# Optimization experiments

Measured on AMD Instinct MI355X. Metric: run time of the kernel, lower is better.

The kernel has to match this reference:

```python
import jax, jax.numpy as jnp
import numpy as np

B, S, D, H, F = 4, 2048, 1024, 16, 4096
HD = D // H
EPS = 1e-6
ROPE_BASE = 10000.0


def apply_rope(x, positions, head_dim):
    # x: [B, S, H, hd], positions: [B, S]
    fraction = 2.0 * jnp.arange(0, head_dim // 2, dtype=jnp.float32) / head_dim
    timescale = ROPE_BASE ** fraction                      # [hd/2]
    angle = positions[:, :, None, None].astype(jnp.float32) / timescale  # [B,S,1,hd/2]
    sin, cos = jnp.sin(angle), jnp.cos(angle)
    first, second = jnp.split(x, 2, axis=-1)
    return jnp.concatenate([first * cos - second * sin,
                            second * cos + first * sin], axis=-1).astype(x.dtype)


def rms_norm(x, scale):
    var = jnp.mean(jnp.square(x), axis=-1, keepdims=True)
    return (x * jax.lax.rsqrt(var + EPS)) * scale


def setup_inputs() -> dict:
    key = jax.random.key(0)
    ks = jax.random.split(key, 10)
    std = 0.02
    x = jax.random.normal(ks[0], (B, S, D), dtype=jnp.float32)
    segment_positions = jnp.broadcast_to(jnp.arange(S, dtype=jnp.int32), (B, S))
    mask = jnp.broadcast_to(jnp.tril(jnp.ones((S, S), dtype=bool))[None, None], (B, 1, S, S))
    wq = jax.random.normal(ks[1], (D, H, HD), dtype=jnp.float32) * std
    wk = jax.random.normal(ks[2], (D, H, HD), dtype=jnp.float32) * std
    wv = jax.random.normal(ks[3], (D, H, HD), dtype=jnp.float32) * std
    wo = jax.random.normal(ks[4], (H, HD, D), dtype=jnp.float32) * std
    w_gate = jax.random.normal(ks[5], (D, F), dtype=jnp.float32) * std
    w_up = jax.random.normal(ks[6], (D, F), dtype=jnp.float32) * std
    w_down = jax.random.normal(ks[7], (F, D), dtype=jnp.float32) * std
    norm1 = jnp.ones((D,), dtype=jnp.float32)
    norm2 = jnp.ones((D,), dtype=jnp.float32)
    return dict(x=x, segment_positions=segment_positions, mask=mask,
                wq=wq, wk=wk, wv=wv, wo=wo,
                w_gate=w_gate, w_up=w_up, w_down=w_down,
                norm1=norm1, norm2=norm2)


def reference(x, segment_positions, mask, wq, wk, wv, wo, w_gate, w_up, w_down, norm1, norm2):
    # --- pre-norm RoPE attention residual block ---
    h = rms_norm(x, norm1)                                  # [B,S,D]
    q = jnp.einsum('bsd,dhk->bshk', h, wq)                  # [B,S,H,hd]
    k = jnp.einsum('bsd,dhk->bshk', h, wk)
    v = jnp.einsum('bsd,dhk->bshk', h, wv)
    q = apply_rope(q, segment_positions, HD)
    k = apply_rope(k, segment_positions, HD)
    q = q / jnp.sqrt(jnp.float32(HD))
    attn = jnp.einsum('bqhd,bkhd->bhqk', q, k)              # [B,H,S,S]
    big_neg = jnp.finfo(jnp.float32).min
    attn = jnp.where(mask, attn, big_neg)
    attn = jax.nn.softmax(attn, axis=-1)
    ctx = jnp.einsum('bhqk,bkhd->bqhd', attn, v)            # [B,S,H,hd]
    x = x + jnp.einsum('bqhd,hdo->bqo', ctx, wo)            # residual
    # --- pre-norm GLU FFN residual block ---
    h = rms_norm(x, norm2)
    gated = jax.nn.gelu(h @ w_gate) * (h @ w_up)            # [B,S,F]
    x = x + gated @ w_down
    return x
```

## Files before the change

kernel.cpp:

```cpp
#include <hip/hip_runtime.h>
#include <cstdint>
#include <cstddef>

#define BQ 4
#define SQ 2048
#define DQ 1024
#define HQ 16
#define HDQ 64
#define FQ 4096
#define MROWS (BQ * SQ)

typedef __attribute__((ext_vector_type(8))) __bf16 bf16x8;
typedef __attribute__((ext_vector_type(8))) unsigned short u16x8;
typedef __attribute__((ext_vector_type(4))) float f32x4;

__device__ __forceinline__ unsigned short f2bf(float f) {
  unsigned int u = __builtin_bit_cast(unsigned int, f);
  u = (u + 0x7FFFu + ((u >> 16) & 1u)) >> 16;
  return (unsigned short)u;
}
__device__ __forceinline__ float bf2f(unsigned short h) {
  unsigned int u = ((unsigned int)h) << 16;
  return __builtin_bit_cast(float, u);
}

typedef const unsigned int __attribute__((address_space(1))) *as1_cu32;
typedef unsigned int __attribute__((address_space(3))) *as3_u32;
#define GLD16(g, l) __builtin_amdgcn_global_load_lds((as1_cu32)(const void*)(g), (as3_u32)(void*)(l), 16, 0, 0)

__global__ __launch_bounds__(256) void k_transpose_bf16(const float* __restrict__ src,
                                                        unsigned short* __restrict__ dst,
                                                        int R, int C) {
  __shared__ float tile[32][33];
  int tx = threadIdx.x & 31, ty = threadIdx.x >> 5;
  int c0 = blockIdx.x * 32, r0 = blockIdx.y * 32;
#pragma unroll
  for (int i = 0; i < 32; i += 8)
    tile[ty + i][tx] = src[(size_t)(r0 + ty + i) * C + (c0 + tx)];
  __syncthreads();
#pragma unroll
  for (int i = 0; i < 32; i += 8)
    dst[(size_t)(c0 + ty + i) * R + (r0 + tx)] = f2bf(tile[tx][ty + i]);
}

__global__ __launch_bounds__(256) void k_rmsnorm(const float* __restrict__ x,
                                                 const float* __restrict__ g,
                                                 unsigned short* __restrict__ out) {
  int row = blockIdx.x, tid = threadIdx.x;
  const float4 v = ((const float4*)(x + (size_t)row * DQ))[tid];
  float ss = v.x * v.x + v.y * v.y + v.z * v.z + v.w * v.w;
#pragma unroll
  for (int d = 32; d >= 1; d >>= 1) ss += __shfl_xor(ss, d);
  __shared__ float ws4[4];
  if ((tid & 63) == 0) ws4[tid >> 6] = ss;
  __syncthreads();
  float tot = ws4[0] + ws4[1] + ws4[2] + ws4[3];
  float r = rsqrtf(tot * (1.0f / DQ) + 1e-6f);
  const float4 gv = ((const float4*)g)[tid];
  ushort4 o;
  o.x = f2bf(v.x * r * gv.x);
  o.y = f2bf(v.y * r * gv.y);
  o.z = f2bf(v.z * r * gv.z);
  o.w = f2bf(v.w * r * gv.w);
  ((ushort4*)(out + (size_t)row * DQ))[tid] = o;
}

template <int MODE>
__global__ __launch_bounds__(256) void k_gemm_bt(const unsigned short* __restrict__ A,
                                                 const unsigned short* __restrict__ Bt,
                                                 void* __restrict__ Cp,
                                                 const float* __restrict__ Res,
                                                 int M, int N, int K) {
  __shared__ __align__(16) unsigned short As[128 * 32];
  __shared__ __align__(16) unsigned short Bs[128 * 32];
  const int tid = threadIdx.x;
  const int lane = tid & 63, w = tid >> 6;
  const int m0 = blockIdx.y * 128, n0 = blockIdx.x * 128;
  const int wm = (w >> 1) * 64, wn = (w & 1) * 64;
  const int lr = lane & 15, lg = lane >> 4;
  f32x4 acc[4][4] = {};
  for (int k0 = 0; k0 < K; k0 += 32) {
#pragma unroll
    for (int i = 0; i < 2; ++i) {
      int flat = i * 256 + tid;
      int row = flat >> 2, ch = flat & 3;
      GLD16(A + (size_t)(m0 + row) * K + k0 + ch * 8, As + (size_t)(i * 256 + w * 64) * 8);
      GLD16(Bt + (size_t)(n0 + row) * K + k0 + ch * 8, Bs + (size_t)(i * 256 + w * 64) * 8);
    }
    __syncthreads();
    bf16x8 af[4], bfr[4];
#pragma unroll
    for (int mi = 0; mi < 4; ++mi)
      af[mi] = *(const bf16x8*)(As + (wm + mi * 16 + lr) * 32 + lg * 8);
#pragma unroll
    for (int ni = 0; ni < 4; ++ni)
      bfr[ni] = *(const bf16x8*)(Bs + (wn + ni * 16 + lr) * 32 + lg * 8);
#pragma unroll
    for (int mi = 0; mi < 4; ++mi)
#pragma unroll
      for (int ni = 0; ni < 4; ++ni)
        acc[mi][ni] = __builtin_amdgcn_mfma_f32_16x16x32_bf16(af[mi], bfr[ni], acc[mi][ni], 0, 0, 0);
    __syncthreads();
  }
#pragma unroll
  for (int mi = 0; mi < 4; ++mi) {
#pragma unroll
    for (int r = 0; r < 4; ++r) {
      int gr = m0 + wm + mi * 16 + lg * 4 + r;
#pragma unroll
      for (int ni = 0; ni < 4; ++ni) {
        int gc = n0 + wn + ni * 16 + lr;
        size_t idx = (size_t)gr * N + gc;
        float v = acc[mi][ni][r];
        if (MODE == 0) {
          ((unsigned short*)Cp)[idx] = f2bf(v);
        } else if (MODE == 1) {
          ((float*)Cp)[idx] = v + Res[idx];
        } else {
          float u = bf2f(((unsigned short*)Cp)[idx]);
          float t = v + 0.044715f * v * v * v;
          float gl = 0.5f * v * (1.0f + tanhf(0.7978845608028654f * t));
          ((unsigned short*)Cp)[idx] = f2bf(gl * u);
        }
      }
    }
  }
}

template <int MODE>
__global__ __launch_bounds__(512, 2) void k_gemm256(const unsigned short* __restrict__ A,
                                                    const unsigned short* __restrict__ Bt,
                                                    void* __restrict__ Cp,
                                                    int M, int N, int K) {
  __shared__ __align__(16) unsigned short Ab[2][2][128 * 64];
  __shared__ __align__(16) unsigned short Bb[2][2][128 * 64];
  const int tid = threadIdx.x, lane = tid & 63, w = tid >> 6;
  const int nwg = (int)gridDim.x;
  const int nx = N >> 8;
  const int cpx = nwg >> 3;
  const int bid = (int)blockIdx.x;
  const int swz = (bid & 7) * cpx + (bid >> 3);
  const int bx = swz % nx, by = swz / nx;
  const int m0 = by * 256, n0 = bx * 256;
  const int wr = (w >> 2) * 128, wc = (w & 3) * 64;
  const int lr = lane & 15, lg = lane >> 4;
  const int NT = K >> 6;
  const int r0 = tid >> 3;
  const int c0sw = (tid & 7) ^ (r0 & 7);
  f32x4 acc[8][4] = {};

#define BAR() asm volatile("s_barrier" ::: "memory")

#define STG(isB, hh_, t_)                                                         \
  do {                                                                            \
    int tpar = (t_) & 1;                                                          \
    int t2 = (t_) > NT - 1 ? NT - 1 : (t_);                                       \
    const unsigned short* gb = (isB) ? Bt : A;                                    \
    int rb = ((isB) ? n0 : m0) + (hh_) * 128;                                     \
    unsigned short* lb =                                                          \
        ((isB) ? &Bb[tpar][hh_][0] : &Ab[tpar][hh_][0]) + (size_t)(w * 64) * 8;   \
    const unsigned short* g0 = gb + (size_t)(rb + r0) * K + t2 * 64 + c0sw * 8;   \
    GLD16(g0, lb);                                                                \
    GLD16(g0 + (size_t)64 * K, lb + 512 * 8);                                     \
  } while (0)

#define RD_A(dst, MH, par)                                                        \
  _Pragma("unroll") for (int mi2 = 0; mi2 < 4; ++mi2) {                           \
    int rr = (wr + ((MH)*4 + mi2) * 16 + lr) & 127;                               \
    int hh = wr >> 7;                                                             \
    _Pragma("unroll") for (int ks = 0; ks < 2; ++ks)                              \
        dst[mi2][ks] =                                                            \
        *(const bf16x8*)&Ab[par][hh][rr * 64 + (((ks * 4 + lg) ^ (rr & 7)) * 8)]; \
  }

#define RD_B(dst, NH, par)                                                        \
  _Pragma("unroll") for (int ni2 = 0; ni2 < 2; ++ni2) {                           \
    int c256 = wc + ((NH)*2 + ni2) * 16 + lr;                                     \
    int hh = c256 >> 7, rr = c256 & 127;                                          \
    _Pragma("unroll") for (int ks = 0; ks < 2; ++ks)                              \
        dst[ni2][ks] =                                                            \
        *(const bf16x8*)&Bb[par][hh][rr * 64 + (((ks * 4 + lg) ^ (rr & 7)) * 8)]; \
  }

#define MM(MH, NH, aqv, bqv)                                                      \
  _Pragma("unroll") for (int mi2 = 0; mi2 < 4; ++mi2)                             \
  _Pragma("unroll") for (int ni2 = 0; ni2 < 2; ++ni2)                             \
  _Pragma("unroll") for (int ks = 0; ks < 2; ++ks)                                \
      acc[(MH)*4 + mi2][(NH)*2 + ni2] = __builtin_amdgcn_mfma_f32_16x16x32_bf16(  \
          aqv[mi2][ks], bqv[ni2][ks], acc[(MH)*4 + mi2][(NH)*2 + ni2], 0, 0, 0);

  STG(0, 0, 0);
  STG(0, 1, 0);
  STG(1, 0, 0);
  STG(1, 1, 0);
  STG(1, 0, 1);
  STG(1, 1, 1);
  asm volatile("s_waitcnt vmcnt(4)" ::: "memory");
  BAR();

  for (int kt = 0; kt < NT; ++kt) {
    const int p = kt & 1;
    bf16x8 aq[4][2], bq0[2][2], bq1[2][2];
    RD_A(aq, 0, p);
    RD_B(bq0, 0, p);
    STG(0, 0, kt + 1);
    BAR();
    __builtin_amdgcn_s_setprio(1);
    MM(0, 0, aq, bq0);
    __builtin_amdgcn_s_setprio(0);
    BAR();
    RD_B(bq1, 1, p);
    STG(0, 1, kt + 1);
    BAR();
    __builtin_amdgcn_s_setprio(1);
    MM(0, 1, aq, bq1);
    __builtin_amdgcn_s_setprio(0);
    BAR();
    RD_A(aq, 1, p);
    STG(1, 0, kt + 2);
    BAR();
    __builtin_amdgcn_s_setprio(1);
    MM(1, 1, aq, bq1);
    __builtin_amdgcn_s_setprio(0);
    BAR();
    STG(1, 1, kt + 2);
    asm volatile("s_waitcnt vmcnt(4)" ::: "memory");
    BAR();
    __builtin_amdgcn_s_setprio(1);
    MM(1, 0, aq, bq0);
    __builtin_amdgcn_s_setprio(0);
    BAR();
  }
  asm volatile("s_waitcnt vmcnt(0)" ::: "memory");
#pragma unroll
  for (int mi = 0; mi < 8; ++mi) {
#pragma unroll
    for (int r = 0; r < 4; ++r) {
      int gr = m0 + wr + mi * 16 + lg * 4 + r;
#pragma unroll
      for (int ni = 0; ni < 4; ++ni) {
        int gc = n0 + wc + ni * 16 + lr;
        size_t idx = (size_t)gr * N + gc;
        float v = acc[mi][ni][r];
        if (MODE == 0) {
          ((unsigned short*)Cp)[idx] = f2bf(v);
        } else {
          float u = bf2f(((unsigned short*)Cp)[idx]);
          float t = v + 0.044715f * v * v * v;
          float gl = 0.5f * v * (1.0f + tanhf(0.7978845608028654f * t));
          ((unsigned short*)Cp)[idx] = f2bf(gl * u);
        }
      }
    }
  }
#undef BAR
#undef STG
#undef RD_A
#undef RD_B
#undef MM
}

__global__ __launch_bounds__(256) void k_rope(const unsigned short* __restrict__ qkv,
                                              const int* __restrict__ pos,
                                              unsigned short* __restrict__ qp,
                                              unsigned short* __restrict__ kp,
                                              unsigned short* __restrict__ vpT) {
  __shared__ unsigned short T[64 * 67];
  const float NEG_L2TS = -0.4152410118609203f;
  const float QSCALE = 0.125f * 1.4426950408889634f;
  int bh = blockIdx.y, b = bh >> 4, hh = bh & 15;
  int s0 = blockIdx.x * 64;
  int tid = threadIdx.x;
  int row = tid >> 2, q4 = tid & 3, j0 = q4 * 8;
  int gs = s0 + row;
  const unsigned short* base = qkv + ((size_t)(b * SQ + gs)) * 3072 + hh * 64;
  u16x8 q1 = *(const u16x8*)(base + j0);
  u16x8 q2 = *(const u16x8*)(base + 32 + j0);
  u16x8 k1 = *(const u16x8*)(base + 1024 + j0);
  u16x8 k2 = *(const u16x8*)(base + 1024 + 32 + j0);
  u16x8 v1 = *(const u16x8*)(base + 2048 + j0);
  u16x8 v2 = *(const u16x8*)(base + 2048 + 32 + j0);
  float fp = (float)pos[b * SQ + gs];
  u16x8 oq1, oq2, ok1, ok2;
#pragma unroll
  for (int jj = 0; jj < 8; ++jj) {
    float ang = fp * exp2f((float)(j0 + jj) * NEG_L2TS);
    float sn, cs;
    __sincosf(ang, &sn, &cs);
    float q1f = bf2f(q1[jj]), q2f = bf2f(q2[jj]);
    float k1f = bf2f(k1[jj]), k2f = bf2f(k2[jj]);
    oq1[jj] = f2bf((q1f * cs - q2f * sn) * QSCALE);
    oq2[jj] = f2bf((q2f * cs + q1f * sn) * QSCALE);
    ok1[jj] = f2bf(k1f * cs - k2f * sn);
    ok2[jj] = f2bf(k2f * cs + k1f * sn);
    T[row * 67 + j0 + jj] = v1[jj];
    T[row * 67 + 32 + j0 + jj] = v2[jj];
  }
  size_t o = ((size_t)bh * SQ + gs) * 64;
  *(u16x8*)(qp + o + j0) = oq1;
  *(u16x8*)(qp + o + 32 + j0) = oq2;
  *(u16x8*)(kp + o + j0) = ok1;
  *(u16x8*)(kp + o + 32 + j0) = ok2;
  __syncthreads();
  int hd = tid >> 2;
#pragma unroll
  for (int c2 = 0; c2 < 2; ++c2) {
    int sb = q4 * 16 + c2 * 8;
    u16x8 ov;
#pragma unroll
    for (int ii = 0; ii < 8; ++ii) ov[ii] = T[(sb + ii) * 67 + hd];
    *(u16x8*)(vpT + ((size_t)bh * 64 + hd) * SQ + s0 + sb) = ov;
  }
}

__global__ __launch_bounds__(256) void k_flash(const unsigned short* __restrict__ qp,
                                               const unsigned short* __restrict__ kp,
                                               const unsigned short* __restrict__ vpT,
                                               unsigned short* __restrict__ ctx) {
  __shared__ __align__(16) unsigned short Ks[2][64 * 64];
  __shared__ __align__(16) unsigned short Vs[2][64 * 64];
  __shared__ __align__(16) unsigned short Ps[4][16 * 64];
  int qb = 31 - (int)blockIdx.x;
  int bh = blockIdx.y, b = bh >> 4, hh = bh & 15;
  int tid = threadIdx.x, lane = tid & 63, w = tid >> 6;
  const int lr = lane & 15, lg = lane >> 4;
  const int key = lr & 7;
  size_t hoff = (size_t)bh * SQ * 64;
  const unsigned short* Q = qp + hoff;
  const unsigned short* Kg = kp + hoff;
  const unsigned short* Vh = vpT + hoff;
  int qr0 = qb * 64 + w * 16;
  bf16x8 aq0 = *(const bf16x8*)(Q + (size_t)(qr0 + lr) * 64 + lg * 8);
  bf16x8 aq1 = *(const bf16x8*)(Q + (size_t)(qr0 + lr) * 64 + 32 + lg * 8);
  f32x4 accO[4] = {};
  float mrow[4] = {-1e30f, -1e30f, -1e30f, -1e30f};
  float lrow[4] = {0.f, 0.f, 0.f, 0.f};
  int nt = qb + 1;

#define STAGE(d, t)                                                              \
  {                                                                              \
    int kv0s = (t) * 64;                                                         \
    _Pragma("unroll") for (int i = 0; i < 2; ++i) {                              \
      int flat = i * 256 + tid;                                                  \
      int srow = flat >> 3;                                                      \
      int ch = (flat & 7) ^ (srow & 7);                                          \
      GLD16(Kg + (size_t)(kv0s + srow) * 64 + ch * 8, &Ks[d][(i * 256 + w * 64) * 8]); \
      GLD16(Vh + (size_t)srow * SQ + kv0s + ch * 8, &Vs[d][(i * 256 + w * 64) * 8]);   \
    }                                                                            \
  }

  STAGE(0, 0);
  __syncthreads();
  for (int t = 0; t < nt; ++t) {
    int kv0 = t * 64;
    if (t + 1 < nt) STAGE((t + 1) & 1, t + 1);
    const unsigned short* Kc = Ks[t & 1];
    const unsigned short* Vc = Vs[t & 1];
    f32x4 sacc[4] = {};
#pragma unroll
    for (int nh = 0; nh < 4; ++nh) {
      const unsigned short* kr = Kc + (nh * 16 + lr) * 64;
      bf16x8 b0 = *(const bf16x8*)(kr + (lg ^ key) * 8);
      bf16x8 b1 = *(const bf16x8*)(kr + ((lg + 4) ^ key) * 8);
      sacc[nh] = __builtin_amdgcn_mfma_f32_16x16x32_bf16(aq0, b0, sacc[nh], 0, 0, 0);
      sacc[nh] = __builtin_amdgcn_mfma_f32_16x16x32_bf16(aq1, b1, sacc[nh], 0, 0, 0);
    }
    bool diag = (t == qb);
    float scl[4];
#pragma unroll
    for (int i = 0; i < 4; ++i) {
      float s0 = sacc[0][i], s1 = sacc[1][i], s2 = sacc[2][i], s3 = sacc[3][i];
      if (diag) {
        int gr = qr0 + lg * 4 + i;
        int c = kv0 + lr;
        if (c > gr) s0 = -1e30f;
        if (c + 16 > gr) s1 = -1e30f;
        if (c + 32 > gr) s2 = -1e30f;
        if (c + 48 > gr) s3 = -1e30f;
      }
      float mt = fmaxf(fmaxf(s0, s1), fmaxf(s2, s3));
      mt = fmaxf(mt, __shfl_xor(mt, 1));
      mt = fmaxf(mt, __shfl_xor(mt, 2));
      mt = fmaxf(mt, __shfl_xor(mt, 4));
      mt = fmaxf(mt, __shfl_xor(mt, 8));
      float mnew = fmaxf(mrow[i], mt);
      scl[i] = exp2f(mrow[i] - mnew);
      mrow[i] = mnew;
      float p0 = exp2f(s0 - mnew), p1 = exp2f(s1 - mnew);
      float p2 = exp2f(s2 - mnew), p3 = exp2f(s3 - mnew);
      lrow[i] = lrow[i] * scl[i] + (p0 + p1 + p2 + p3);
      int prow = lg * 4 + i;
      unsigned short* Pr = &Ps[w][prow * 64];
      int pk = prow & 7;
      int sub = lr >> 3, off = lr & 7;
      Pr[((0 + sub) ^ pk) * 8 + off] = f2bf(p0);
      Pr[((2 + sub) ^ pk) * 8 + off] = f2bf(p1);
      Pr[((4 + sub) ^ pk) * 8 + off] = f2bf(p2);
      Pr[((6 + sub) ^ pk) * 8 + off] = f2bf(p3);
    }
#pragma unroll
    for (int n2 = 0; n2 < 4; ++n2)
#pragma unroll
      for (int i = 0; i < 4; ++i) accO[n2][i] *= scl[i];
    bf16x8 ap0 = *(const bf16x8*)(&Ps[w][lr * 64] + (lg ^ key) * 8);
    bf16x8 ap1 = *(const bf16x8*)(&Ps[w][lr * 64] + ((lg + 4) ^ key) * 8);
#pragma unroll
    for (int n2 = 0; n2 < 4; ++n2) {
      const unsigned short* vr = Vc + (n2 * 16 + lr) * 64;
      bf16x8 bv0 = *(const bf16x8*)(vr + (lg ^ key) * 8);
      bf16x8 bv1 = *(const bf16x8*)(vr + ((lg + 4) ^ key) * 8);
      accO[n2] = __builtin_amdgcn_mfma_f32_16x16x32_bf16(ap0, bv0, accO[n2], 0, 0, 0);
      accO[n2] = __builtin_amdgcn_mfma_f32_16x16x32_bf16(ap1, bv1, accO[n2], 0, 0, 0);
    }
    __syncthreads();
  }
#pragma unroll
  for (int i = 0; i < 4; ++i) {
    float l = lrow[i];
    l += __shfl_xor(l, 1);
    l += __shfl_xor(l, 2);
    l += __shfl_xor(l, 4);
    l += __shfl_xor(l, 8);
    lrow[i] = 1.0f / l;
  }
#pragma unroll
  for (int n2 = 0; n2 < 4; ++n2)
#pragma unroll
    for (int i = 0; i < 4; ++i) {
      int gs = qr0 + lg * 4 + i;
      ctx[((size_t)b * SQ + gs) * DQ + hh * 64 + n2 * 16 + lr] = f2bf(accO[n2][i] * lrow[i]);
    }
#undef STAGE
}

extern "C" void kernel_launch(void* const* d_in, const int* in_sizes, int n_in,
                              void* d_out, int out_size, void* d_ws, size_t ws_size,
                              hipStream_t stream) {
  (void)in_sizes; (void)n_in; (void)out_size; (void)ws_size;
  const float* x   = (const float*)d_in[0];
  const int*   pos = (const int*)d_in[1];
  const float* wq  = (const float*)d_in[3];
  const float* wk  = (const float*)d_in[4];
  const float* wv  = (const float*)d_in[5];
  const float* wo  = (const float*)d_in[6];
  const float* wg  = (const float*)d_in[7];
  const float* wu  = (const float*)d_in[8];
  const float* wd  = (const float*)d_in[9];
  const float* n1  = (const float*)d_in[10];
  const float* n2v = (const float*)d_in[11];
  char* ws = (char*)d_ws;
  const size_t MB = 1024ull * 1024ull;
  unsigned short* qkvT  = (unsigned short*)(ws);
  unsigned short* woT   = (unsigned short*)(ws + 6 * MB);
  unsigned short* gateT = (unsigned short*)(ws + 8 * MB);
  unsigned short* upT   = (unsigned short*)(ws + 16 * MB);
  unsigned short* downT = (unsigned short*)(ws + 24 * MB);
  unsigned short* qkv   = (unsigned short*)(ws + 32 * MB);
  unsigned short* act   = qkv;
  unsigned short* qpb   = (unsigned short*)(ws + 80 * MB);
  unsigned short* kpb   = (unsigned short*)(ws + 96 * MB);
  unsigned short* vpT   = (unsigned short*)(ws + 112 * MB);
  unsigned short* hbuf  = (unsigned short*)(ws + 128 * MB);
  unsigned short* ctx   = hbuf;
  float*          x2    = (float*)(ws + 144 * MB);
  unsigned short* h2    = (unsigned short*)(ws + 176 * MB);
  float*          out   = (float*)d_out;

  dim3 b256(256);
  k_transpose_bf16<<<dim3(32, 32), b256, 0, stream>>>(wq, qkvT, 1024, 1024);
  k_transpose_bf16<<<dim3(32, 32), b256, 0, stream>>>(wk, qkvT + 1024 * 1024, 1024, 1024);
  k_transpose_bf16<<<dim3(32, 32), b256, 0, stream>>>(wv, qkvT + 2 * 1024 * 1024, 1024, 1024);
  k_transpose_bf16<<<dim3(32, 32), b256, 0, stream>>>(wo, woT, 1024, 1024);
  k_transpose_bf16<<<dim3(128, 32), b256, 0, stream>>>(wg, gateT, 1024, 4096);
  k_transpose_bf16<<<dim3(128, 32), b256, 0, stream>>>(wu, upT, 1024, 4096);
  k_transpose_bf16<<<dim3(32, 128), b256, 0, stream>>>(wd, downT, 4096, 1024);
  k_rmsnorm<<<MROWS, b256, 0, stream>>>(x, n1, hbuf);
  k_gemm256<0><<<dim3(384), dim3(512), 0, stream>>>(hbuf, qkvT, qkv, MROWS, 3072, 1024);
  k_rope<<<dim3(32, 64), b256, 0, stream>>>(qkv, pos, qpb, kpb, vpT);
  k_flash<<<dim3(32, 64), b256, 0, stream>>>(qpb, kpb, vpT, ctx);
  k_gemm_bt<1><<<dim3(8, 64), b256, 0, stream>>>(ctx, woT, x2, x, MROWS, 1024, 1024);
  k_rmsnorm<<<MROWS, b256, 0, stream>>>(x2, n2v, h2);
  k_gemm256<0><<<dim3(512), dim3(512), 0, stream>>>(h2, upT, act, MROWS, 4096, 1024);
  k_gemm256<2><<<dim3(512), dim3(512), 0, stream>>>(h2, gateT, act, MROWS, 4096, 1024);
  k_gemm_bt<1><<<dim3(8, 64), b256, 0, stream>>>(act, downT, out, x2, MROWS, 1024, 4096);
}
```

Before: 830.4 us.

## Double flash-attention query tile per block and cheapen GELU epilogue

The flash kernel now gives each wave 32 query rows, so a block covers 128 rows. Each K/V tile staged in shared memory is reused across twice as many queries, and the grid is halved. Waves whose rows lie entirely above a KV tile skip its compute. GELU's tanh is rewritten as a sigmoid form using exp2 and a fast reciprocal, and P is rounded to bf16 by truncation. This lowers load traffic and transcendental cost, but uses more registers, gives fewer blocks for load balance, and loses a little accuracy.

Result: no change. 814.4 us (-1.9%).

```diff
diff --git a/kernel.cpp b/kernel.cpp
--- a/kernel.cpp
+++ b/kernel.cpp
@@ -19,9 +19,17 @@
   u = (u + 0x7FFFu + ((u >> 16) & 1u)) >> 16;
   return (unsigned short)u;
 }
+__device__ __forceinline__ unsigned short f2bf_trunc(float f) {
+  return (unsigned short)(__builtin_bit_cast(unsigned int, f) >> 16);
+}
 __device__ __forceinline__ float bf2f(unsigned short h) {
   unsigned int u = ((unsigned int)h) << 16;
   return __builtin_bit_cast(float, u);
+}
+__device__ __forceinline__ float gelu_f(float v) {
+  float t = v + 0.044715f * v * v * v;
+  float e = exp2f(-2.3022082299f * t);
+  return v * __builtin_amdgcn_rcpf(1.0f + e);
 }
 
 typedef const unsigned int __attribute__((address_space(1))) *as1_cu32;
@@ -118,9 +126,7 @@
           ((float*)Cp)[idx] = v + Res[idx];
         } else {
           float u = bf2f(((unsigned short*)Cp)[idx]);
-          float t = v + 0.044715f * v * v * v;
-          float gl = 0.5f * v * (1.0f + tanhf(0.7978845608028654f * t));
-          ((unsigned short*)Cp)[idx] = f2bf(gl * u);
+          ((unsigned short*)Cp)[idx] = f2bf(gelu_f(v) * u);
         }
       }
     }
@@ -246,9 +252,7 @@
           ((unsigned short*)Cp)[idx] = f2bf(v);
         } else {
           float u = bf2f(((unsigned short*)Cp)[idx]);
-          float t = v + 0.044715f * v * v * v;
-          float gl = 0.5f * v * (1.0f + tanhf(0.7978845608028654f * t));
-          ((unsigned short*)Cp)[idx] = f2bf(gl * u);
+          ((unsigned short*)Cp)[idx] = f2bf(gelu_f(v) * u);
         }
       }
     }
@@ -313,14 +317,14 @@
   }
 }
 
-__global__ __launch_bounds__(256) void k_flash(const unsigned short* __restrict__ qp,
-                                               const unsigned short* __restrict__ kp,
-                                               const unsigned short* __restrict__ vpT,
-                                               unsigned short* __restrict__ ctx) {
+__global__ __launch_bounds__(256, 3) void k_flash(const unsigned short* __restrict__ qp,
+                                                  const unsigned short* __restrict__ kp,
+                                                  const unsigned short* __restrict__ vpT,
+                                                  unsigned short* __restrict__ ctx) {
   __shared__ __align__(16) unsigned short Ks[2][64 * 64];
   __shared__ __align__(16) unsigned short Vs[2][64 * 64];
-  __shared__ __align__(16) unsigned short Ps[4][16 * 64];
-  int qb = 31 - (int)blockIdx.x;
+  __shared__ __align__(16) unsigned short Ps[4][32 * 64];
+  int qb = 15 - (int)blockIdx.x;
   int bh = blockIdx.y, b = bh >> 4, hh = bh & 15;
   int tid = threadIdx.x, lane = tid & 63, w = tid >> 6;
   const int lr = lane & 15, lg = lane >> 4;
@@ -329,13 +333,20 @@
   const unsigned short* Q = qp + hoff;
   const unsigned short* Kg = kp + hoff;
   const unsigned short* Vh = vpT + hoff;
-  int qr0 = qb * 64 + w * 16;
-  bf16x8 aq0 = *(const bf16x8*)(Q + (size_t)(qr0 + lr) * 64 + lg * 8);
-  bf16x8 aq1 = *(const bf16x8*)(Q + (size_t)(qr0 + lr) * 64 + 32 + lg * 8);
-  f32x4 accO[4] = {};
-  float mrow[4] = {-1e30f, -1e30f, -1e30f, -1e30f};
-  float lrow[4] = {0.f, 0.f, 0.f, 0.f};
-  int nt = qb + 1;
+  int qr0 = qb * 128 + w * 32;
+  bf16x8 aq[2][2];
+#pragma unroll
+  for (int mi = 0; mi < 2; ++mi) {
+    aq[mi][0] = *(const bf16x8*)(Q + (size_t)(qr0 + mi * 16 + lr) * 64 + lg * 8);
+    aq[mi][1] = *(const bf16x8*)(Q + (size_t)(qr0 + mi * 16 + lr) * 64 + 32 + lg * 8);
+  }
+  f32x4 accO[2][4] = {};
+  float mrow[2][4], lrow[2][4];
+#pragma unroll
+  for (int mi = 0; mi < 2; ++mi)
+#pragma unroll
+    for (int i = 0; i < 4; ++i) { mrow[mi][i] = -1e30f; lrow[mi][i] = 0.f; }
+  int nt = qb * 2 + 2;
 
 #define STAGE(d, t)                                                              \
   {                                                                              \
@@ -356,80 +367,101 @@
     if (t + 1 < nt) STAGE((t + 1) & 1, t + 1);
     const unsigned short* Kc = Ks[t & 1];
     const unsigned short* Vc = Vs[t & 1];
-    f32x4 sacc[4] = {};
-#pragma unroll
-    for (int nh = 0; nh < 4; ++nh) {
-      const unsigned short* kr = Kc + (nh * 16 + lr) * 64;
-      bf16x8 b0 = *(const bf16x8*)(kr + (lg ^ key) * 8);
-      bf16x8 b1 = *(const bf16x8*)(kr + ((lg + 4) ^ key) * 8);
-      sacc[nh] = __builtin_amdgcn_mfma_f32_16x16x32_bf16(aq0, b0, sacc[nh], 0, 0, 0);
-      sacc[nh] = __builtin_amdgcn_mfma_f32_16x16x32_bf16(aq1, b1, sacc[nh], 0, 0, 0);
-    }
-    bool diag = (t == qb);
-    float scl[4];
-#pragma unroll
-    for (int i = 0; i < 4; ++i) {
-      float s0 = sacc[0][i], s1 = sacc[1][i], s2 = sacc[2][i], s3 = sacc[3][i];
-      if (diag) {
-        int gr = qr0 + lg * 4 + i;
-        int c = kv0 + lr;
-        if (c > gr) s0 = -1e30f;
-        if (c + 16 > gr) s1 = -1e30f;
-        if (c + 32 > gr) s2 = -1e30f;
-        if (c + 48 > gr) s3 = -1e30f;
-      }
-      float mt = fmaxf(fmaxf(s0, s1), fmaxf(s2, s3));
-      mt = fmaxf(mt, __shfl_xor(mt, 1));
-      mt = fmaxf(mt, __shfl_xor(mt, 2));
-      mt = fmaxf(mt, __shfl_xor(mt, 4));
-      mt = fmaxf(mt, __shfl_xor(mt, 8));
-      float mnew = fmaxf(mrow[i], mt);
-      scl[i] = exp2f(mrow[i] - mnew);
-      mrow[i] = mnew;
-      float p0 = exp2f(s0 - mnew), p1 = exp2f(s1 - mnew);
-      float p2 = exp2f(s2 - mnew), p3 = exp2f(s3 - mnew);
-      lrow[i] = lrow[i] * scl[i] + (p0 + p1 + p2 + p3);
-      int prow = lg * 4 + i;
-      unsigned short* Pr = &Ps[w][prow * 64];
-      int pk = prow & 7;
-      int sub = lr >> 3, off = lr & 7;
-      Pr[((0 + sub) ^ pk) * 8 + off] = f2bf(p0);
-      Pr[((2 + sub) ^ pk) * 8 + off] = f2bf(p1);
-      Pr[((4 + sub) ^ pk) * 8 + off] = f2bf(p2);
-      Pr[((6 + sub) ^ pk) * 8 + off] = f2bf(p3);
-    }
-#pragma unroll
-    for (int n2 = 0; n2 < 4; ++n2)
-#pragma unroll
-      for (int i = 0; i < 4; ++i) accO[n2][i] *= scl[i];
-    bf16x8 ap0 = *(const bf16x8*)(&Ps[w][lr * 64] + (lg ^ key) * 8);
-    bf16x8 ap1 = *(const bf16x8*)(&Ps[w][lr * 64] + ((lg + 4) ^ key) * 8);
-#pragma unroll
-    for (int n2 = 0; n2 < 4; ++n2) {
-      const unsigned short* vr = Vc + (n2 * 16 + lr) * 64;
-      bf16x8 bv0 = *(const bf16x8*)(vr + (lg ^ key) * 8);
-      bf16x8 bv1 = *(const bf16x8*)(vr + ((lg + 4) ^ key) * 8);
-      accO[n2] = __builtin_amdgcn_mfma_f32_16x16x32_bf16(ap0, bv0, accO[n2], 0, 0, 0);
-      accO[n2] = __builtin_amdgcn_mfma_f32_16x16x32_bf16(ap1, bv1, accO[n2], 0, 0, 0);
+    bool active = (kv0 <= qr0 + 31);
+    if (active) {
+      f32x4 sacc[2][4] = {};
+#pragma unroll
+      for (int nh = 0; nh < 4; ++nh) {
+        const unsigned short* kr = Kc + (nh * 16 + lr) * 64;
+        bf16x8 b0 = *(const bf16x8*)(kr + (lg ^ key) * 8);
+        bf16x8 b1 = *(const bf16x8*)(kr + ((lg + 4) ^ key) * 8);
+#pragma unroll
+        for (int mi = 0; mi < 2; ++mi) {
+          sacc[mi][nh] = __builtin_amdgcn_mfma_f32_16x16x32_bf16(aq[mi][0], b0, sacc[mi][nh], 0, 0, 0);
+          sacc[mi][nh] = __builtin_amdgcn_mfma_f32_16x16x32_bf16(aq[mi][1], b1, sacc[mi][nh], 0, 0, 0);
+        }
+      }
+      bool diag = (kv0 + 63 > qr0);
+      float scl[2][4];
+#pragma unroll
+      for (int mi = 0; mi < 2; ++mi) {
+#pragma unroll
+        for (int i = 0; i < 4; ++i) {
+          float s0 = sacc[mi][0][i], s1 = sacc[mi][1][i], s2 = sacc[mi][2][i], s3 = sacc[mi][3][i];
+          if (diag) {
+            int gr = qr0 + mi * 16 + lg * 4 + i;
+            int c = kv0 + lr;
+            if (c > gr) s0 = -1e30f;
+            if (c + 16 > gr) s1 = -1e30f;
+            if (c + 32 > gr) s2 = -1e30f;
+            if (c + 48 > gr) s3 = -1e30f;
+          }
+          float mt = fmaxf(fmaxf(s0, s1), fmaxf(s2, s3));
+          mt = fmaxf(mt, __shfl_xor(mt, 1));
+          mt = fmaxf(mt, __shfl_xor(mt, 2));
+          mt = fmaxf(mt, __shfl_xor(mt, 4));
+          mt = fmaxf(mt, __shfl_xor(mt, 8));
+          float mnew = fmaxf(mrow[mi][i], mt);
+          scl[mi][i] = exp2f(mrow[mi][i] - mnew);
+          mrow[mi][i] = mnew;
+          float p0 = exp2f(s0 - mnew), p1 = exp2f(s1 - mnew);
+          float p2 = exp2f(s2 - mnew), p3 = exp2f(s3 - mnew);
+          lrow[mi][i] = lrow[mi][i] * scl[mi][i] + (p0 + p1 + p2 + p3);
+          int prow = mi * 16 + lg * 4 + i;
+          unsigned short* Pr = &Ps[w][prow * 64];
+          int pk = prow & 7;
+          int sub = lr >> 3, off = lr & 7;
+          Pr[((0 + sub) ^ pk) * 8 + off] = f2bf_trunc(p0);
+          Pr[((2 + sub) ^ pk) * 8 + off] = f2bf_trunc(p1);
+          Pr[((4 + sub) ^ pk) * 8 + off] = f2bf_trunc(p2);
+          Pr[((6 + sub) ^ pk) * 8 + off] = f2bf_trunc(p3);
+        }
+#pragma unroll
+        for (int n2 = 0; n2 < 4; ++n2)
+#pragma unroll
+          for (int i = 0; i < 4; ++i) accO[mi][n2][i] *= scl[mi][i];
+      }
+      bf16x8 ap[2][2];
+#pragma unroll
+      for (int mi = 0; mi < 2; ++mi) {
+        const unsigned short* pr = &Ps[w][(mi * 16 + lr) * 64];
+        ap[mi][0] = *(const bf16x8*)(pr + (lg ^ key) * 8);
+        ap[mi][1] = *(const bf16x8*)(pr + ((lg + 4) ^ key) * 8);
+      }
+#pragma unroll
+      for (int n2 = 0; n2 < 4; ++n2) {
+        const unsigned short* vr = Vc + (n2 * 16 + lr) * 64;
+        bf16x8 bv0 = *(const bf16x8*)(vr + (lg ^ key) * 8);
+        bf16x8 bv1 = *(const bf16x8*)(vr + ((lg + 4) ^ key) * 8);
+#pragma unroll
+        for (int mi = 0; mi < 2; ++mi) {
+          accO[mi][n2] = __builtin_amdgcn_mfma_f32_16x16x32_bf16(ap[mi][0], bv0, accO[mi][n2], 0, 0, 0);
+          accO[mi][n2] = __builtin_amdgcn_mfma_f32_16x16x32_bf16(ap[mi][1], bv1, accO[mi][n2], 0, 0, 0);
+        }
+      }
     }
     __syncthreads();
   }
 #pragma unroll
-  for (int i = 0; i < 4; ++i) {
-    float l = lrow[i];
-    l += __shfl_xor(l, 1);
-    l += __shfl_xor(l, 2);
-    l += __shfl_xor(l, 4);
-    l += __shfl_xor(l, 8);
-    lrow[i] = 1.0f / l;
-  }
-#pragma unroll
-  for (int n2 = 0; n2 < 4; ++n2)
+  for (int mi = 0; mi < 2; ++mi)
 #pragma unroll
     for (int i = 0; i < 4; ++i) {
-      int gs = qr0 + lg * 4 + i;
-      ctx[((size_t)b * SQ + gs) * DQ + hh * 64 + n2 * 16 + lr] = f2bf(accO[n2][i] * lrow[i]);
+      float l = lrow[mi][i];
+      l += __shfl_xor(l, 1);
+      l += __shfl_xor(l, 2);
+      l += __shfl_xor(l, 4);
+      l += __shfl_xor(l, 8);
+      lrow[mi][i] = 1.0f / l;
     }
+#pragma unroll
+  for (int mi = 0; mi < 2; ++mi)
+#pragma unroll
+    for (int n2 = 0; n2 < 4; ++n2)
+#pragma unroll
+      for (int i = 0; i < 4; ++i) {
+        int gs = qr0 + mi * 16 + lg * 4 + i;
+        ctx[((size_t)b * SQ + gs) * DQ + hh * 64 + n2 * 16 + lr] = f2bf(accO[mi][n2][i] * lrow[mi][i]);
+      }
 #undef STAGE
 }
 
@@ -477,7 +509,7 @@
   k_rmsnorm<<<MROWS, b256, 0, stream>>>(x, n1, hbuf);
   k_gemm256<0><<<dim3(384), dim3(512), 0, stream>>>(hbuf, qkvT, qkv, MROWS, 3072, 1024);
   k_rope<<<dim3(32, 64), b256, 0, stream>>>(qkv, pos, qpb, kpb, vpT);
-  k_flash<<<dim3(32, 64), b256, 0, stream>>>(qpb, kpb, vpT, ctx);
+  k_flash<<<dim3(16, 64), b256, 0, stream>>>(qpb, kpb, vpT, ctx);
   k_gemm_bt<1><<<dim3(8, 64), b256, 0, stream>>>(ctx, woT, x2, x, MROWS, 1024, 1024);
   k_rmsnorm<<<MROWS, b256, 0, stream>>>(x2, n2v, h2);
   k_gemm256<0><<<dim3(512), dim3(512), 0, stream>>>(h2, upT, act, MROWS, 4096, 1024);
```
